# Kernel tuning notes

Measured on AMD Instinct MI355X. Metric: run time of the kernel, lower is better.

The kernel has to match this reference:

```python
import jax, jax.numpy as jnp
import numpy as np

DEPTH = 10
N_LEAF = 1024        # = n_nodes = 2**DEPTH
FEATURE_LENGTH = 1024
BATCH = 16384


def setup_inputs() -> dict:
    key = jax.random.key(0)
    kx, kidx, kw, kb = jax.random.split(key, 4)
    x = jax.random.normal(kx, (BATCH, FEATURE_LENGTH), dtype=jnp.float32)
    # feature_mask: one-hot column selection, onehot[using_idx].T -> [feature_length, n_leaf]
    using_idx = jax.random.randint(kidx, (N_LEAF,), 0, FEATURE_LENGTH)
    feature_mask = jax.nn.one_hot(using_idx, FEATURE_LENGTH, dtype=jnp.float32).T
    # n_nodes tiny Linear(n_leaf, 1) layers batched into one [n_leaf, n_nodes] weight
    W = jax.random.normal(kw, (N_LEAF, N_LEAF), dtype=jnp.float32) / np.sqrt(N_LEAF)
    b = jax.random.normal(kb, (N_LEAF,), dtype=jnp.float32) * 0.01
    return {"x": x, "feature_mask": feature_mask, "W": W, "b": b}


def reference(x, feature_mask, W, b):
    B = x.shape[0]
    feats = x @ feature_mask                      # [B, n_leaf]
    d = jax.nn.sigmoid(feats @ W + b)             # [B, n_nodes] (all node linears as one GEMM)
    decision = jnp.stack([d, 1.0 - d], axis=-1)   # [B, n_nodes, 2]
    mu = jnp.ones((B, 1), dtype=x.dtype)
    parts = [jnp.ones((B, 2), dtype=x.dtype)]     # initial big_mu of ones
    begin = 1                                     # node 0 is unused, matching original indexing
    for n_layer in range(DEPTH):
        n = 2 ** n_layer
        nd = decision[:, begin:begin + n, :]      # [B, n, 2]
        mu = (mu[:, :, None] * nd).reshape(B, 2 * n)
        parts.append(mu)
        begin += n
    return jnp.concatenate(parts, axis=1)         # [B, 2 + (2**(DEPTH+1) - 2)] = [B, 2048]
```

## Files before the change

### kernel.cpp

```cpp
#include <hip/hip_runtime.h>


typedef __bf16 bf16x8 __attribute__((ext_vector_type(8)));
typedef float  f32x4  __attribute__((ext_vector_type(4)));

#define BATCH 16384
#define NLEAF 1024
#define FEAT  1024
#define OUTC  2048

__device__ __forceinline__ unsigned short f2bf(float f) {
    union { float f; unsigned int u; } c; c.f = f;
    unsigned int u = c.u;
    u += 0x7FFFu + ((u >> 16) & 1u);
    return (unsigned short)(u >> 16);
}

__device__ __forceinline__ float bf2f(unsigned short u) {
    union { unsigned int i; float f; } c; c.i = (unsigned int)u << 16;
    return c.f;
}

__device__ __forceinline__ void load_lds16(const void* g, void* l) {
    __builtin_amdgcn_global_load_lds(
        (const __attribute__((address_space(1))) unsigned int*)g,
        (__attribute__((address_space(3))) unsigned int*)l, 16, 0, 0);
}

__device__ __forceinline__ float sigmoidf(float z) {
    return 1.0f / (1.0f + __expf(-z));
}

__global__ __launch_bounds__(256) void prep_w(const float* __restrict__ fm,
                                              const float* __restrict__ W,
                                              int* __restrict__ idx,
                                              short* __restrict__ Wt) {
    __shared__ short tile[64][65];
    const int b = blockIdx.x, t = threadIdx.x;
    if (b < 1024) {
        const int f = b;
#pragma unroll
        for (int i = 0; i < 4; ++i) {
            int leaf = i * 256 + t;
            if (fm[(size_t)f * NLEAF + leaf] > 0.5f) idx[leaf] = f;
        }
    } else {
        const int tb = b - 1024;
        const int k0 = (tb >> 4) * 64, n0 = (tb & 15) * 64;
#pragma unroll
        for (int i = 0; i < 16; ++i) {
            int e = i * 256 + t;
            int kr = e >> 6, nc = e & 63;
            tile[kr][nc] = (short)f2bf(W[(size_t)(k0 + kr) * NLEAF + n0 + nc]);
        }
        __syncthreads();
#pragma unroll
        for (int i = 0; i < 16; ++i) {
            int e = i * 256 + t;
            int nr = e >> 6, kc = e & 63;
            Wt[(size_t)(n0 + nr) * FEAT + k0 + kc] = tile[kc][nr];
        }
    }
}

__global__ __launch_bounds__(256) void gather_feats(const float* __restrict__ x,
                                                    const int* __restrict__ idx,
                                                    short* __restrict__ feats) {
    __shared__ float xs[8][1024];
    __shared__ int   ids[1024];
    const int t = threadIdx.x;
    const int r0 = blockIdx.x * 8;

    {
        int4 v = ((const int4*)idx)[t];
        *(int4*)&ids[t * 4] = v;
    }
#pragma unroll
    for (int j = 0; j < 8; ++j) {
        int e = j * 256 + t;
        int row = e >> 8, c4 = e & 255;
        ((float4*)xs[row])[c4] =
            ((const float4*)(x + (size_t)(r0 + row) * FEAT))[c4];
    }
    __syncthreads();

#pragma unroll
    for (int j = 0; j < 4; ++j) {
        int e = j * 256 + t;
        int row = e >> 7, kk = (e & 127) * 8;
        union { short s[8]; int4 v; } pk;
#pragma unroll
        for (int q = 0; q < 8; ++q)
            pk.s[q] = (short)f2bf(xs[row][ids[kk + q]]);
        *(int4*)(feats + (size_t)(r0 + row) * FEAT + kk) = pk.v;
    }
}


#define STAGEH(P, TT, BUFN)                                                   \
    {                                                                         \
        constexpr int hh = (P) & 1;                                           \
        _Pragma("unroll")                                                     \
        for (int j = 0; j < 2; ++j) {                                         \
            const int r = j * 64 + r8;                                        \
            if ((P) < 2) {                                                    \
                load_lds16(feats + (size_t)(row0 + hh * 128 + r) * FEAT       \
                               + ((TT) << 6) + (ss << 3),                     \
                           smem + (BUFN) * 32768 + hh * 16384                 \
                               + (j * 512 + tid) * 16);                       \
            } else {                                                          \
                load_lds16(Wt + (size_t)(n0 + hh * 128 + r) * FEAT            \
                               + ((TT) << 6) + (ss << 3),                     \
                           smem + 65536 + (BUFN) * 32768 + hh * 16384         \
                               + (j * 512 + tid) * 16);                       \
            }                                                                 \
        }                                                                     \
    }

#define GPHASE(P, DO_STAGE, DO_WAITV)                                         \
    {                                                                         \
        constexpr int qm = (P) >> 1, qn = (P) & 1;                            \
        bf16x8 av[4][2], bv[2][2];                                            \
        _Pragma("unroll")                                                     \
        for (int mm = 0; mm < 4; ++mm)                                        \
            _Pragma("unroll")                                                 \
            for (int kh = 0; kh < 2; ++kh)                                    \
                av[mm][kh] = *(const bf16x8*)(smem + bufA                     \
                               + aRow[qm * 4 + mm] + slotoff[kh]);            \
        _Pragma("unroll")                                                     \
        for (int nn = 0; nn < 2; ++nn)                                        \
            _Pragma("unroll")                                                 \
            for (int kh = 0; kh < 2; ++kh)                                    \
                bv[nn][kh] = *(const bf16x8*)(smem + bufA                     \
                               + bRow[qn * 2 + nn] + slotoff[kh]);            \
        if (DO_STAGE) STAGEH(P, t + 1, bufN);                                 \
        __builtin_amdgcn_s_barrier();                                         \
        asm volatile("s_waitcnt lgkmcnt(0)" ::: "memory");                    \
        __builtin_amdgcn_sched_barrier(0);                                    \
        __builtin_amdgcn_s_setprio(1);                                        \
        _Pragma("unroll")                                                     \
        for (int mm = 0; mm < 4; ++mm)                                        \
            _Pragma("unroll")                                                 \
            for (int nn = 0; nn < 2; ++nn)                                    \
                _Pragma("unroll")                                             \
                for (int kh = 0; kh < 2; ++kh)                                \
                    acc[qm * 4 + mm][qn * 2 + nn] =                           \
                        __builtin_amdgcn_mfma_f32_16x16x32_bf16(              \
                            av[mm][kh], bv[nn][kh],                           \
                            acc[qm * 4 + mm][qn * 2 + nn], 0, 0, 0);          \
        __builtin_amdgcn_s_setprio(0);                                        \
        if (DO_WAITV) { asm volatile("s_waitcnt vmcnt(0)" ::: "memory"); }    \
        __builtin_amdgcn_s_barrier();                                         \
    }

__global__ __launch_bounds__(512, 2) void gemm256_sig_d(
        const short* __restrict__ feats, const short* __restrict__ Wt,
        const float* __restrict__ bias, unsigned short* __restrict__ dout) {
    __shared__ __align__(16) char smem_[131072];
    char* smem = smem_;

    const int tid = threadIdx.x, l = tid & 63, w = tid >> 6;
    const int wr = w >> 2, wc = w & 3;
    const int lr = l & 15, lk = l >> 4;
    const int bid = blockIdx.x;
    const int swz = (bid & 7) * 32 + (bid >> 3);
    const int row0 = (swz >> 2) << 8;
    const int n0   = (swz & 3) << 8;

    const int r8 = tid >> 3;
    const int ss = (tid & 7) ^ (r8 & 7);

    int aRow[8], bRow[4], slotoff[2];
#pragma unroll
    for (int m = 0; m < 8; ++m)
        aRow[m] = wr * 16384 + (m * 16 + lr) * 128;
#pragma unroll
    for (int n = 0; n < 4; ++n)
        bRow[n] = 65536 + (wc >> 1) * 16384 + ((wc & 1) * 64 + n * 16 + lr) * 128;
#pragma unroll
    for (int kh = 0; kh < 2; ++kh)
        slotoff[kh] = ((kh * 4 + lk) ^ (lr & 7)) * 16;

    float bvreg[4];
#pragma unroll
    for (int n = 0; n < 4; ++n)
        bvreg[n] = bias[n0 + wc * 64 + n * 16 + lr];

    f32x4 acc[8][4];
#pragma unroll
    for (int m = 0; m < 8; ++m)
#pragma unroll
        for (int n = 0; n < 4; ++n)
#pragma unroll
            for (int r = 0; r < 4; ++r) acc[m][n][r] = 0.0f;

    STAGEH(0, 0, 0);
    STAGEH(1, 0, 0);
    STAGEH(2, 0, 0);
    STAGEH(3, 0, 0);
    asm volatile("s_waitcnt vmcnt(0)" ::: "memory");
    __builtin_amdgcn_s_barrier();

    for (int t = 0; t < 16; ++t) {
        const int bufA = (t & 1) * 32768;
        const int bufN = (t & 1) ^ 1;
        const bool st = (t < 15);
        GPHASE(0, st, false);
        GPHASE(1, st, false);
        GPHASE(2, st, false);
        GPHASE(3, st, st);
    }

#pragma unroll
    for (int m = 0; m < 8; ++m) {
#pragma unroll
        for (int n = 0; n < 4; ++n) {
            const int col = n0 + wc * 64 + n * 16 + lr;
#pragma unroll
            for (int rr = 0; rr < 4; ++rr) {
                const int row = row0 + wr * 128 + m * 16 + lk * 4 + rr;
                dout[(size_t)row * 4096 + 3072 + col] =
                    f2bf(sigmoidf(acc[m][n][rr] + bvreg[n]));
            }
        }
    }
}

__global__ __launch_bounds__(256) void expand_tree(float* __restrict__ out) {
    const int t = threadIdx.x, l = t & 63, w = t >> 6;
    const int row = blockIdx.x * 4 + w;
    const unsigned short* dr =
        (const unsigned short*)out + (size_t)row * 4096 + 3072;
    float* orow = out + (size_t)row * OUTC;

    float dpath[6];
#pragma unroll
    for (int j = 0; j <= 5; ++j) {
        int idx = l >> (5 - j);
        dpath[j] = bf2f(dr[(1 << j) + (idx >> 1)]);
    }
    float d6 = bf2f(dr[64 + l]);
    unsigned int u7 = *(const unsigned int*)(dr + 128 + 2 * l);
    float d7[2] = { bf2f((unsigned short)(u7 & 0xffff)),
                    bf2f((unsigned short)(u7 >> 16)) };
    uint2 u8 = *(const uint2*)(dr + 256 + 4 * l);
    float d8[4] = { bf2f((unsigned short)(u8.x & 0xffff)),
                    bf2f((unsigned short)(u8.x >> 16)),
                    bf2f((unsigned short)(u8.y & 0xffff)),
                    bf2f((unsigned short)(u8.y >> 16)) };
    uint4 u9 = *(const uint4*)(dr + 512 + 8 * l);
    float d9[8] = { bf2f((unsigned short)(u9.x & 0xffff)),
                    bf2f((unsigned short)(u9.x >> 16)),
                    bf2f((unsigned short)(u9.y & 0xffff)),
                    bf2f((unsigned short)(u9.y >> 16)),
                    bf2f((unsigned short)(u9.z & 0xffff)),
                    bf2f((unsigned short)(u9.z >> 16)),
                    bf2f((unsigned short)(u9.w & 0xffff)),
                    bf2f((unsigned short)(u9.w >> 16)) };

    float p = 1.0f;
#pragma unroll
    for (int j = 0; j <= 5; ++j) {
        int idx = l >> (5 - j);
        p *= (idx & 1) ? (1.0f - dpath[j]) : dpath[j];
        if ((l & ((1 << (5 - j)) - 1)) == 0)
            orow[(2 << j) + idx] = p;
    }
    if (l < 2) orow[l] = 1.0f;

    float v6[2] = { p * d6, p * (1.0f - d6) };
    *(float2*)(orow + 128 + 2 * l) = make_float2(v6[0], v6[1]);

    float v7[4];
#pragma unroll
    for (int e = 0; e < 4; ++e)
        v7[e] = v6[e >> 1] * ((e & 1) ? (1.0f - d7[e >> 1]) : d7[e >> 1]);
    *(float4*)(orow + 256 + 4 * l) = make_float4(v7[0], v7[1], v7[2], v7[3]);

    float v8[8];
#pragma unroll
    for (int e = 0; e < 8; ++e)
        v8[e] = v7[e >> 1] * ((e & 1) ? (1.0f - d8[e >> 1]) : d8[e >> 1]);
    *(float4*)(orow + 512 + 8 * l)     = make_float4(v8[0], v8[1], v8[2], v8[3]);
    *(float4*)(orow + 512 + 8 * l + 4) = make_float4(v8[4], v8[5], v8[6], v8[7]);

    float v9[16];
#pragma unroll
    for (int e = 0; e < 16; ++e)
        v9[e] = v8[e >> 1] * ((e & 1) ? (1.0f - d9[e >> 1]) : d9[e >> 1]);
#pragma unroll
    for (int q = 0; q < 4; ++q)
        *(float4*)(orow + 1024 + 16 * l + 4 * q) =
            make_float4(v9[4*q], v9[4*q+1], v9[4*q+2], v9[4*q+3]);
}

template <bool HAS_IDX>
__global__ __launch_bounds__(256) void fused_naive(const float* __restrict__ x,
                                                   const float* __restrict__ fm,
                                                   const float* __restrict__ W,
                                                   const float* __restrict__ bias,
                                                   const int* __restrict__ idx,
                                                   float* __restrict__ out) {
    __shared__ float fx[1024];
    __shared__ float dsm[1024];
    __shared__ float tre[2048];
    __shared__ int   idl[1024];
    const int t = threadIdx.x;
    const int row = blockIdx.x;

    if (HAS_IDX) {
        for (int k = t; k < 1024; k += 256) idl[k] = idx[k];
    } else {
        for (int k = t; k < 1024; k += 256) {
            int found = 0;
            for (int f = 0; f < 1024; ++f)
                if (fm[(size_t)f * NLEAF + k] > 0.5f) found = f;
            idl[k] = found;
        }
    }
    __syncthreads();
    const float* xr = x + (size_t)row * FEAT;
    for (int k = t; k < 1024; k += 256) fx[k] = xr[idl[k]];
    __syncthreads();

    float a0 = 0.f, a1 = 0.f, a2 = 0.f, a3 = 0.f;
    for (int k = 0; k < 1024; ++k) {
        float f = fx[k];
        const float* wrp = W + (size_t)k * NLEAF + t;
        a0 = fmaf(f, wrp[0],   a0);
        a1 = fmaf(f, wrp[256], a1);
        a2 = fmaf(f, wrp[512], a2);
        a3 = fmaf(f, wrp[768], a3);
    }
    dsm[t]       = sigmoidf(a0 + bias[t]);
    dsm[t + 256] = sigmoidf(a1 + bias[t + 256]);
    dsm[t + 512] = sigmoidf(a2 + bias[t + 512]);
    dsm[t + 768] = sigmoidf(a3 + bias[t + 768]);
    if (t < 2) tre[t] = 1.0f;
    __syncthreads();

    for (int L = 0; L < 10; ++L) {
        int n = 2 << L;
        for (int k = t; k < n; k += 256) {
            int node = (1 << L) + (k >> 1);
            float dv = dsm[node];
            tre[n + k] = tre[node] * ((k & 1) ? (1.0f - dv) : dv);
        }
        __syncthreads();
    }
    float4* orow = (float4*)(out + (size_t)row * OUTC);
    const float4* ts = (const float4*)tre;
    for (int i = t; i < 512; i += 256) orow[i] = ts[i];
}

extern "C" void kernel_launch(void* const* d_in, const int* in_sizes, int n_in,
                              void* d_out, int out_size, void* d_ws, size_t ws_size,
                              hipStream_t stream) {
    const float* x    = (const float*)d_in[0];
    const float* fm   = (const float*)d_in[1];
    const float* W    = (const float*)d_in[2];
    const float* bias = (const float*)d_in[3];
    float* out = (float*)d_out;

    const size_t IDX_B   = 4096;
    const size_t WT_B    = (size_t)NLEAF * FEAT * 2;
    const size_t FEATS_B = (size_t)BATCH * FEAT * 2;
    const size_t need = IDX_B + WT_B + FEATS_B;

    if (ws_size >= need) {
        int*   idx   = (int*)d_ws;
        short* Wt    = (short*)((char*)d_ws + IDX_B);
        short* feats = (short*)((char*)d_ws + IDX_B + WT_B);

        prep_w<<<1280, 256, 0, stream>>>(fm, W, idx, Wt);
        gather_feats<<<BATCH / 8, 256, 0, stream>>>(x, idx, feats);
        gemm256_sig_d<<<(BATCH / 256) * (NLEAF / 256), 512, 0, stream>>>(
            feats, Wt, bias, (unsigned short*)out);
        expand_tree<<<BATCH / 4, 256, 0, stream>>>(out);
    } else if (ws_size >= IDX_B) {
        int* idx = (int*)d_ws;
        prep_w<<<1280, 256, 0, stream>>>(fm, nullptr, idx, nullptr);
        fused_naive<true><<<BATCH, 256, 0, stream>>>(x, fm, W, bias, idx, out);
    } else {
        fused_naive<false><<<BATCH, 256, 0, stream>>>(x, fm, W, bias, nullptr, out);
    }
}
```

Measured before the change: 101.5 us.

## Split GEMM K-tile into halves with finer-grained vmcnt waits and new LDS layout

Reorganizes the bf16 GEMM main loop so each 64-wide K tile is staged and consumed as two 32-wide halves, with separate LDS regions and a new XOR swizzle. Phases now iterate over M quarter and K half, loading B fragments once per K half and reusing them across both M quarters. Uses partial vmcnt(4) waits so the second K half's loads can still be in flight while the first half is computed. This aims to cut LDS reads per MFMA and expose more load/compute overlap, at the cost of more complex synchronization and a peeled final iteration.

New measurement: 97.53 us. 3.9% less time.

```diff
diff --git a/kernel.cpp b/kernel.cpp
--- a/kernel.cpp
+++ b/kernel.cpp
@@ -97,43 +97,34 @@
 }
 
 
-#define STAGEH(P, TT, BUFN)                                                   \
+#define STAGEH(MAT, KH, TT, BUFN)                                             \
     {                                                                         \
-        constexpr int hh = (P) & 1;                                           \
         _Pragma("unroll")                                                     \
         for (int j = 0; j < 2; ++j) {                                         \
-            const int r = j * 64 + r8;                                        \
-            if ((P) < 2) {                                                    \
-                load_lds16(feats + (size_t)(row0 + hh * 128 + r) * FEAT       \
-                               + ((TT) << 6) + (ss << 3),                     \
-                           smem + (BUFN) * 32768 + hh * 16384                 \
-                               + (j * 512 + tid) * 16);                       \
-            } else {                                                          \
-                load_lds16(Wt + (size_t)(n0 + hh * 128 + r) * FEAT            \
-                               + ((TT) << 6) + (ss << 3),                     \
-                           smem + 65536 + (BUFN) * 32768 + hh * 16384         \
-                               + (j * 512 + tid) * 16);                       \
-            }                                                                 \
+            const int slotidx = j * 512 + tid;                                \
+            const int srow = slotidx >> 2;                                    \
+            const short* srcb = (MAT) ? (Wt + (size_t)(n0 + srow) * FEAT)     \
+                                      : (feats + (size_t)(row0 + srow) * FEAT);\
+            load_lds16(srcb + ((TT) << 6) + ((KH) << 5) + (ssrc << 3),        \
+                       smem + (MAT) * 65536 + (BUFN) * 32768                  \
+                            + (KH) * 16384 + slotidx * 16);                   \
         }                                                                     \
     }
 
-#define GPHASE(P, DO_STAGE, DO_WAITV)                                         \
+#define GPHASE(QM, KH, DO_STAGE, SMAT, SKH, WAITV)                            \
     {                                                                         \
-        constexpr int qm = (P) >> 1, qn = (P) & 1;                            \
-        bf16x8 av[4][2], bv[2][2];                                            \
+        bf16x8 av[4];                                                         \
         _Pragma("unroll")                                                     \
         for (int mm = 0; mm < 4; ++mm)                                        \
+            av[mm] = *(const bf16x8*)(smem + bufA + (KH) * 16384              \
+                                      + aRow[(QM) * 4 + mm]);                 \
+        if ((QM) == 0) {                                                      \
             _Pragma("unroll")                                                 \
-            for (int kh = 0; kh < 2; ++kh)                                    \
-                av[mm][kh] = *(const bf16x8*)(smem + bufA                     \
-                               + aRow[qm * 4 + mm] + slotoff[kh]);            \
-        _Pragma("unroll")                                                     \
-        for (int nn = 0; nn < 2; ++nn)                                        \
-            _Pragma("unroll")                                                 \
-            for (int kh = 0; kh < 2; ++kh)                                    \
-                bv[nn][kh] = *(const bf16x8*)(smem + bufA                     \
-                               + bRow[qn * 2 + nn] + slotoff[kh]);            \
-        if (DO_STAGE) STAGEH(P, t + 1, bufN);                                 \
+            for (int nn = 0; nn < 4; ++nn)                                    \
+                bvk[nn] = *(const bf16x8*)(smem + bufA + (KH) * 16384         \
+                                           + bRow[nn]);                       \
+        }                                                                     \
+        if (DO_STAGE) STAGEH(SMAT, SKH, t + 1, bufN);                         \
         __builtin_amdgcn_s_barrier();                                         \
         asm volatile("s_waitcnt lgkmcnt(0)" ::: "memory");                    \
         __builtin_amdgcn_sched_barrier(0);                                    \
@@ -141,15 +132,13 @@
         _Pragma("unroll")                                                     \
         for (int mm = 0; mm < 4; ++mm)                                        \
             _Pragma("unroll")                                                 \
-            for (int nn = 0; nn < 2; ++nn)                                    \
-                _Pragma("unroll")                                             \
-                for (int kh = 0; kh < 2; ++kh)                                \
-                    acc[qm * 4 + mm][qn * 2 + nn] =                           \
-                        __builtin_amdgcn_mfma_f32_16x16x32_bf16(              \
-                            av[mm][kh], bv[nn][kh],                           \
-                            acc[qm * 4 + mm][qn * 2 + nn], 0, 0, 0);          \
+            for (int nn = 0; nn < 4; ++nn)                                    \
+                acc[(QM) * 4 + mm][nn] =                                      \
+                    __builtin_amdgcn_mfma_f32_16x16x32_bf16(                  \
+                        av[mm], bvk[nn], acc[(QM) * 4 + mm][nn], 0, 0, 0);    \
         __builtin_amdgcn_s_setprio(0);                                        \
-        if (DO_WAITV) { asm volatile("s_waitcnt vmcnt(0)" ::: "memory"); }    \
+        if ((WAITV) == 1) { asm volatile("s_waitcnt vmcnt(4)" ::: "memory"); }\
+        if ((WAITV) == 2) { asm volatile("s_waitcnt vmcnt(0)" ::: "memory"); }\
         __builtin_amdgcn_s_barrier();                                         \
     }
 
@@ -167,19 +156,16 @@
     const int row0 = (swz >> 2) << 8;
     const int n0   = (swz & 3) << 8;
 
-    const int r8 = tid >> 3;
-    const int ss = (tid & 7) ^ (r8 & 7);
-
-    int aRow[8], bRow[4], slotoff[2];
+    const int ssrc = (tid & 3) ^ ((tid >> 3) & 3);
+
+    const int slotoff = (lk ^ ((lr >> 1) & 3)) << 4;
+    int aRow[8], bRow[4];
 #pragma unroll
     for (int m = 0; m < 8; ++m)
-        aRow[m] = wr * 16384 + (m * 16 + lr) * 128;
+        aRow[m] = (wr * 128 + m * 16 + lr) * 64 + slotoff;
 #pragma unroll
     for (int n = 0; n < 4; ++n)
-        bRow[n] = 65536 + (wc >> 1) * 16384 + ((wc & 1) * 64 + n * 16 + lr) * 128;
-#pragma unroll
-    for (int kh = 0; kh < 2; ++kh)
-        slotoff[kh] = ((kh * 4 + lk) ^ (lr & 7)) * 16;
+        bRow[n] = 65536 + (wc * 64 + n * 16 + lr) * 64 + slotoff;
 
     float bvreg[4];
 #pragma unroll
@@ -194,21 +180,33 @@
 #pragma unroll
             for (int r = 0; r < 4; ++r) acc[m][n][r] = 0.0f;
 
-    STAGEH(0, 0, 0);
-    STAGEH(1, 0, 0);
-    STAGEH(2, 0, 0);
-    STAGEH(3, 0, 0);
-    asm volatile("s_waitcnt vmcnt(0)" ::: "memory");
+    {
+        const int t = -1, bufN = 0;
+        STAGEH(0, 0, t + 1, bufN);
+        STAGEH(1, 0, t + 1, bufN);
+        STAGEH(0, 1, t + 1, bufN);
+        STAGEH(1, 1, t + 1, bufN);
+    }
+    asm volatile("s_waitcnt vmcnt(4)" ::: "memory");
     __builtin_amdgcn_s_barrier();
 
-    for (int t = 0; t < 16; ++t) {
+    bf16x8 bvk[4];
+    for (int t = 0; t < 15; ++t) {
         const int bufA = (t & 1) * 32768;
         const int bufN = (t & 1) ^ 1;
-        const bool st = (t < 15);
-        GPHASE(0, st, false);
-        GPHASE(1, st, false);
-        GPHASE(2, st, false);
-        GPHASE(3, st, st);
+        GPHASE(0, 0, true, 0, 0, 0);
+        GPHASE(1, 0, true, 1, 0, 1);
+        GPHASE(0, 1, true, 0, 1, 0);
+        GPHASE(1, 1, true, 1, 1, 1);
+    }
+    {
+        const int t = 15;
+        const int bufA = 32768, bufN = 0;
+        (void)bufN;
+        GPHASE(0, 0, false, 0, 0, 0);
+        GPHASE(1, 0, false, 1, 0, 2);
+        GPHASE(0, 1, false, 0, 1, 0);
+        GPHASE(1, 1, false, 1, 1, 0);
     }
 
 #pragma unroll
```
